# Kernel optimization log

Measured on AMD Instinct MI355X. Metric: run time of the kernel, lower is better.

Reference implementation:

```python
import jax, jax.numpy as jnp
import numpy as np

KB, KI = 6, 0   # kernel quantizer: quantized_bits(6, 0, alpha=1)
BB, BI = 6, 0   # bias quantizer:   quantized_bits(6, 0, alpha=1)
AB, AI = 6, 0   # activation:       quantized_relu(6, 0)


def _round_ste(p):
    # straight-through round (QKeras _round_through); tf.round and jnp.round
    # both round half-to-even
    return p + jax.lax.stop_gradient(jnp.round(p) - p)


def quantized_bits(x, bits, integer):
    # QKeras quantized_bits with keep_negative=1, symmetric=0, alpha=1
    m = float(2 ** (bits - 1))      # non-sign levels
    m_i = float(2 ** integer)
    p = x * (m / m_i)
    return (m_i / m) * jnp.clip(_round_ste(p), -m, m - 1.0)


def quantized_relu(x, bits, integer):
    # QKeras quantized_relu with negative_slope=0, use_sigmoid=0
    m = float(2 ** bits)
    m_i = float(2 ** integer)
    p = x * (m / m_i)
    return (m_i / m) * jnp.clip(_round_ste(p), 0.0, m - 1.0)


def setup_inputs() -> dict:
    key = jax.random.key(0)
    ks = jax.random.split(key, 9)
    dims = [128, 1024, 2048, 4096, 4096]
    inp = {"x": jax.random.normal(ks[0], (8192, dims[0]), dtype=jnp.float32)}
    for i in range(4):
        fan_in, fan_out = dims[i], dims[i + 1]
        scale = np.sqrt(2.0 / (fan_in + fan_out))  # glorot-ish scale
        inp[f"W{i}"] = jax.random.normal(ks[1 + 2 * i], (fan_in, fan_out), dtype=jnp.float32) * scale
        inp[f"b{i}"] = jax.random.normal(ks[2 + 2 * i], (fan_out,), dtype=jnp.float32) * 0.01
    return inp


def reference(x, W0, b0, W1, b1, W2, b2, W3, b3):
    Ws = [W0, W1, W2, W3]
    bs = [b0, b1, b2, b3]
    h = x
    for i in range(4):
        wq = quantized_bits(Ws[i], KB, KI)
        bq = quantized_bits(bs[i], BB, BI)
        h = jnp.dot(h, wq) + bq
        if i != 3:  # last layer has activation=None
            h = quantized_relu(h, AB, AI)
    return h
```

## Files before the change

### kernel.cpp

```cpp
#include <hip/hip_runtime.h>
#include <stdint.h>

typedef int v4i __attribute__((ext_vector_type(4)));

__device__ __forceinline__ float qlevel(float x) {
  float p = rintf(x * 32.0f);
  return fminf(fmaxf(p, -32.0f), 31.0f);
}

__device__ __forceinline__ int8_t qrelu_level(float p) {
  int q = (int)rintf(p);
  q = q < 0 ? 0 : (q > 63 ? 63 : q);
  return (int8_t)q;
}

__device__ __forceinline__ void async16(const void* g, void* l) {
  __builtin_amdgcn_global_load_lds(
      (const __attribute__((address_space(1))) void*)g,
      (__attribute__((address_space(3))) void*)l, 16, 0, 0);
}

__global__ __launch_bounds__(256) void quant_w0_k(const float* __restrict__ W,
                                                  int8_t* __restrict__ wq) {
  int i = blockIdx.x * 256 + threadIdx.x;
  float4 v = ((const float4*)W)[i];
  char4 c;
  c.x = (int8_t)(int)qlevel(v.x);
  c.y = (int8_t)(int)qlevel(v.y);
  c.z = (int8_t)(int)qlevel(v.z);
  c.w = (int8_t)(int)qlevel(v.w);
  ((char4*)wq)[i] = c;
}

__global__ __launch_bounds__(256) void quantT_k(const float* __restrict__ W,
                                                int8_t* __restrict__ wt,
                                                int K, int N) {
  const int t = threadIdx.x;
  const int l = t & 63;
  const int kc = t >> 6;
  const int k0 = blockIdx.y * 64 + kc * 16;
  const int n = blockIdx.x * 64 + l;
  union { int8_t b[16]; int4 v; } u;
#pragma unroll
  for (int j = 0; j < 16; ++j)
    u.b[j] = (int8_t)(int)qlevel(W[(size_t)(k0 + j) * N + n]);
  *(int4*)&wt[(size_t)n * K + k0] = u.v;
}

__global__ __launch_bounds__(256) void quant_bias_k(
    const float* __restrict__ b0, const float* __restrict__ b1,
    const float* __restrict__ b2, const float* __restrict__ b3,
    float* __restrict__ o0, float* __restrict__ o1,
    float* __restrict__ o2, float* __restrict__ o3) {
  int i = blockIdx.x * 256 + threadIdx.x;
  if (i < 1024) o0[i] = qlevel(b0[i]);
  if (i < 2048) o1[i] = qlevel(b1[i]);
  o2[i] = qlevel(b2[i]);
  o3[i] = qlevel(b3[i]);
}

__global__ __launch_bounds__(256) void layer0_k(const float* __restrict__ x,
                                                const int8_t* __restrict__ w0q,
                                                const float* __restrict__ bint,
                                                int8_t* __restrict__ a1) {
  const int K = 128, N = 1024;
  __shared__ float xs[64][132];
  __shared__ int8_t wsm[128][64];
  const int tid = threadIdx.x;
  const int m0 = blockIdx.y * 64;
  const int n0 = blockIdx.x * 64;
#pragma unroll
  for (int i = 0; i < 8; ++i) {
    int idx = tid + 256 * i;
    int row = idx >> 5, c4 = idx & 31;
    float4 v = *(const float4*)(x + (size_t)(m0 + row) * K + c4 * 4);
    *(float4*)&xs[row][c4 * 4] = v;
  }
#pragma unroll
  for (int i = 0; i < 8; ++i) {
    int idx = tid + 256 * i;
    int k = idx >> 4, c4 = idx & 15;
    *(int*)&wsm[k][c4 * 4] = *(const int*)(w0q + (size_t)k * N + n0 + c4 * 4);
  }
  __syncthreads();
  const int ty = tid >> 4, tx = tid & 15;
  float acc[4][4] = {};
  for (int k4 = 0; k4 < K; k4 += 4) {
    float xr[4][4];
#pragma unroll
    for (int i = 0; i < 4; ++i) {
      float4 v = *(const float4*)&xs[ty * 4 + i][k4];
      xr[i][0] = v.x; xr[i][1] = v.y; xr[i][2] = v.z; xr[i][3] = v.w;
    }
#pragma unroll
    for (int kk = 0; kk < 4; ++kk) {
      char4 cv = *(const char4*)&wsm[k4 + kk][tx * 4];
      float w0 = (float)cv.x, w1 = (float)cv.y, w2 = (float)cv.z, w3 = (float)cv.w;
#pragma unroll
      for (int i = 0; i < 4; ++i) {
        acc[i][0] = fmaf(xr[i][kk], w0, acc[i][0]);
        acc[i][1] = fmaf(xr[i][kk], w1, acc[i][1]);
        acc[i][2] = fmaf(xr[i][kk], w2, acc[i][2]);
        acc[i][3] = fmaf(xr[i][kk], w3, acc[i][3]);
      }
    }
  }
  const int n = n0 + tx * 4;
  float b0v = 2.0f * bint[n + 0], b1v = 2.0f * bint[n + 1];
  float b2v = 2.0f * bint[n + 2], b3v = 2.0f * bint[n + 3];
#pragma unroll
  for (int i = 0; i < 4; ++i) {
    int m = m0 + ty * 4 + i;
    char4 o;
    o.x = qrelu_level(2.0f * acc[i][0] + b0v);
    o.y = qrelu_level(2.0f * acc[i][1] + b1v);
    o.z = qrelu_level(2.0f * acc[i][2] + b2v);
    o.w = qrelu_level(2.0f * acc[i][3] + b3v);
    *(char4*)&a1[(size_t)m * 1024 + n] = o;
  }
}

template <bool FINAL>
__global__ __launch_bounds__(512) void gemm_i8(const int8_t* __restrict__ A,
                                               const int8_t* __restrict__ BT,
                                               const float* __restrict__ bint,
                                               void* __restrict__ outp,
                                               int M, int N, int K) {
  __shared__ __align__(16) int8_t ldsA[3][256 * 64];
  __shared__ __align__(16) int8_t ldsB[3][256 * 64];
  const int tid = threadIdx.x;
  const int wid = tid >> 6;
  const int lane = tid & 63;
  const int wm = wid >> 2, wn = wid & 3;
  const int quad = lane >> 4, r = lane & 15;
  const int m0 = blockIdx.y * 256, n0 = blockIdx.x * 256;

  const int8_t* Ab = A + (size_t)m0 * K;
  const int8_t* Bb = BT + (size_t)n0 * K;

  const int srow = tid >> 2;
  const int sp = tid & 3;
  const int skc = (sp - (srow >> 1)) & 3;
  const int8_t* gA0 = Ab + (size_t)srow * K + skc * 16;
  const int8_t* gA1 = Ab + (size_t)(srow + 128) * K + skc * 16;
  const int8_t* gB0 = Bb + (size_t)srow * K + skc * 16;
  const int8_t* gB1 = Bb + (size_t)(srow + 128) * K + skc * 16;
  const int ldsOff0 = (wid * 64) * 16;
  const int ldsOff1 = (512 + wid * 64) * 16;

  const int pfrag = (quad + (r >> 1)) & 3;

  v4i acc[8][4] = {};

#define STAGE_A(buf, kt)                              \
  do {                                                \
    async16(gA0 + (kt) * 64, &ldsA[buf][ldsOff0]);    \
    async16(gA1 + (kt) * 64, &ldsA[buf][ldsOff1]);    \
  } while (0)
#define STAGE_B(buf, kt)                              \
  do {                                                \
    async16(gB0 + (kt) * 64, &ldsB[buf][ldsOff0]);    \
    async16(gB1 + (kt) * 64, &ldsB[buf][ldsOff1]);    \
  } while (0)

#define ITER(p, q, kt, doStage, vmN)                                          \
  do {                                                                        \
    v4i bf[4], af[4];                                                         \
    const int8_t* La_ = &ldsA[p][0];                                          \
    const int8_t* Lb_ = &ldsB[p][0];                                          \
    _Pragma("unroll")                                                         \
    for (int nt = 0; nt < 4; ++nt)                                            \
      bf[nt] = *(const v4i*)&Lb_[(wn * 64 + nt * 16 + r) * 64 + pfrag * 16];  \
    _Pragma("unroll")                                                         \
    for (int mt = 0; mt < 4; ++mt)                                            \
      af[mt] = *(const v4i*)&La_[(wm * 128 + mt * 16 + r) * 64 + pfrag * 16]; \
    if (doStage) STAGE_A(q, kt);                                              \
    __builtin_amdgcn_s_barrier();                                             \
    asm volatile("s_waitcnt lgkmcnt(0)" ::: "memory");                        \
    __builtin_amdgcn_sched_barrier(0);                                        \
    __builtin_amdgcn_s_setprio(1);                                            \
    _Pragma("unroll")                                                         \
    for (int mt = 0; mt < 4; ++mt)                                            \
      _Pragma("unroll")                                                       \
      for (int nt = 0; nt < 4; ++nt)                                          \
        acc[mt][nt] = __builtin_amdgcn_mfma_i32_16x16x64_i8(                  \
            af[mt], bf[nt], acc[mt][nt], 0, 0, 0);                            \
    __builtin_amdgcn_s_setprio(0);                                            \
    __builtin_amdgcn_s_barrier();                                             \
    _Pragma("unroll")                                                         \
    for (int mt = 0; mt < 4; ++mt)                                            \
      af[mt] = *(const v4i*)&La_[(wm * 128 + 64 + mt * 16 + r) * 64 +         \
                                 pfrag * 16];                                 \
    if (doStage) STAGE_B(q, kt);                                              \
    if (vmN == 4) asm volatile("s_waitcnt vmcnt(4)" ::: "memory");            \
    if (vmN == 0) asm volatile("s_waitcnt vmcnt(0)" ::: "memory");            \
    __builtin_amdgcn_s_barrier();                                             \
    asm volatile("s_waitcnt lgkmcnt(0)" ::: "memory");                        \
    __builtin_amdgcn_sched_barrier(0);                                        \
    __builtin_amdgcn_s_setprio(1);                                            \
    _Pragma("unroll")                                                         \
    for (int mt = 0; mt < 4; ++mt)                                            \
      _Pragma("unroll")                                                       \
      for (int nt = 0; nt < 4; ++nt)                                          \
        acc[4 + mt][nt] = __builtin_amdgcn_mfma_i32_16x16x64_i8(              \
            af[mt], bf[nt], acc[4 + mt][nt], 0, 0, 0);                        \
    __builtin_amdgcn_s_setprio(0);                                            \
    __builtin_amdgcn_s_barrier();                                             \
  } while (0)

  const int NT = K >> 6;

  STAGE_A(0, 0); STAGE_B(0, 0);
  STAGE_A(1, 1); STAGE_B(1, 1);
  asm volatile("s_waitcnt vmcnt(4)" ::: "memory");
  __builtin_amdgcn_s_barrier();

  for (int t = 0; t < NT - 2; ++t) {
    ITER(t % 3, (t + 2) % 3, t + 2, true, 4);
  }
  ITER((NT - 2) % 3, 0, 0, false, 0);
  ITER((NT - 1) % 3, 0, 0, false, -1);

#undef ITER
#undef STAGE_A
#undef STAGE_B

  const int mbase = m0 + wm * 128;
  const int nbase = n0 + wn * 64;
  if (FINAL) {
    float* out = (float*)outp;
#pragma unroll
    for (int nt = 0; nt < 4; ++nt) {
      int n = nbase + nt * 16 + r;
      float bq = bint[n] * 0.03125f;
#pragma unroll
      for (int mt = 0; mt < 8; ++mt)
#pragma unroll
        for (int g = 0; g < 4; ++g) {
          int m = mbase + mt * 16 + quad * 4 + g;
          out[(size_t)m * N + n] = (float)acc[mt][nt][g] * (1.0f / 2048.0f) + bq;
        }
    }
  } else {
    int8_t* out = (int8_t*)outp;
#pragma unroll
    for (int nt = 0; nt < 4; ++nt) {
      int n = nbase + nt * 16 + r;
      float b2 = 2.0f * bint[n];
#pragma unroll
      for (int mt = 0; mt < 8; ++mt)
#pragma unroll
        for (int g = 0; g < 4; ++g) {
          int m = mbase + mt * 16 + quad * 4 + g;
          out[(size_t)m * N + n] =
              qrelu_level((float)acc[mt][nt][g] * 0.03125f + b2);
        }
    }
  }
}

extern "C" void kernel_launch(void* const* d_in, const int* in_sizes, int n_in,
                              void* d_out, int out_size, void* d_ws, size_t ws_size,
                              hipStream_t stream) {
  const float* x  = (const float*)d_in[0];
  const float* W0 = (const float*)d_in[1];
  const float* b0 = (const float*)d_in[2];
  const float* W1 = (const float*)d_in[3];
  const float* b1 = (const float*)d_in[4];
  const float* W2 = (const float*)d_in[5];
  const float* b2 = (const float*)d_in[6];
  const float* W3 = (const float*)d_in[7];
  const float* b3 = (const float*)d_in[8];

  uint8_t* ws = (uint8_t*)d_ws;
  int8_t* wq0 = (int8_t*)(ws + 0);
  int8_t* wt1 = (int8_t*)(ws + 131072);
  int8_t* wt2 = (int8_t*)(ws + 2228224);
  int8_t* wt3 = (int8_t*)(ws + 10616832);
  float*  bq0 = (float*)(ws + 27394048);
  float*  bq1 = (float*)(ws + 27398144);
  float*  bq2 = (float*)(ws + 27406336);
  float*  bq3 = (float*)(ws + 27422720);
  int8_t* a1  = (int8_t*)(ws + 27439104);
  int8_t* a2  = (int8_t*)(ws + 35827712);
  int8_t* a3  = (int8_t*)(ws + 52604928);

  quant_w0_k<<<128, 256, 0, stream>>>(W0, wq0);
  quantT_k<<<dim3(2048 / 64, 1024 / 64), 256, 0, stream>>>(W1, wt1, 1024, 2048);
  quantT_k<<<dim3(4096 / 64, 2048 / 64), 256, 0, stream>>>(W2, wt2, 2048, 4096);
  quantT_k<<<dim3(4096 / 64, 4096 / 64), 256, 0, stream>>>(W3, wt3, 4096, 4096);
  quant_bias_k<<<16, 256, 0, stream>>>(b0, b1, b2, b3, bq0, bq1, bq2, bq3);
  layer0_k<<<dim3(16, 128), 256, 0, stream>>>(x, wq0, bq0, a1);
  gemm_i8<false><<<dim3(2048 / 256, 8192 / 256), 512, 0, stream>>>(
      a1, wt1, bq1, a2, 8192, 2048, 1024);
  gemm_i8<false><<<dim3(4096 / 256, 8192 / 256), 512, 0, stream>>>(
      a2, wt2, bq2, a3, 8192, 4096, 2048);
  gemm_i8<true><<<dim3(4096 / 256, 8192 / 256), 512, 0, stream>>>(
      a3, wt3, bq3, d_out, 8192, 4096, 4096);
}
```

Before: 492.6 us.

## Collapse per-iteration barriers into one barrier and load all A fragments upfront

Each k-step of the int8 MFMA GEMM main loop now runs behind a single barrier instead of four. All eight A fragments and the four B fragments are read from LDS before any MFMA, and the A and B async global-to-LDS copies for the next stage are issued together. The explicit lgkmcnt waits and sched_barriers go away, so the compiler places the LDS waits and can overlap the LDS reads with the MFMAs. The goal is to cut barrier stalls and wave synchronisation per k-step. The cost is extra registers for the second A fragment set and less explicit control over where instructions are scheduled.

```diff
diff --git a/kernel.cpp b/kernel.cpp
--- a/kernel.cpp
+++ b/kernel.cpp
@@ -152,20 +152,18 @@
 
   v4i acc[8][4] = {};
 
-#define STAGE_A(buf, kt)                              \
+#define STAGE(buf, kt)                                \
   do {                                                \
     async16(gA0 + (kt) * 64, &ldsA[buf][ldsOff0]);    \
     async16(gA1 + (kt) * 64, &ldsA[buf][ldsOff1]);    \
-  } while (0)
-#define STAGE_B(buf, kt)                              \
-  do {                                                \
     async16(gB0 + (kt) * 64, &ldsB[buf][ldsOff0]);    \
     async16(gB1 + (kt) * 64, &ldsB[buf][ldsOff1]);    \
   } while (0)
 
 #define ITER(p, q, kt, doStage, vmN)                                          \
   do {                                                                        \
-    v4i bf[4], af[4];                                                         \
+    __builtin_amdgcn_s_barrier();                                             \
+    v4i bf[4], af0[4], af1[4];                                                \
     const int8_t* La_ = &ldsA[p][0];                                          \
     const int8_t* Lb_ = &ldsB[p][0];                                          \
     _Pragma("unroll")                                                         \
@@ -173,47 +171,35 @@
       bf[nt] = *(const v4i*)&Lb_[(wn * 64 + nt * 16 + r) * 64 + pfrag * 16];  \
     _Pragma("unroll")                                                         \
     for (int mt = 0; mt < 4; ++mt)                                            \
-      af[mt] = *(const v4i*)&La_[(wm * 128 + mt * 16 + r) * 64 + pfrag * 16]; \
-    if (doStage) STAGE_A(q, kt);                                              \
-    __builtin_amdgcn_s_barrier();                                             \
-    asm volatile("s_waitcnt lgkmcnt(0)" ::: "memory");                        \
-    __builtin_amdgcn_sched_barrier(0);                                        \
+      af0[mt] = *(const v4i*)&La_[(wm * 128 + mt * 16 + r) * 64 + pfrag * 16];\
+    _Pragma("unroll")                                                         \
+    for (int mt = 0; mt < 4; ++mt)                                            \
+      af1[mt] = *(const v4i*)&La_[(wm * 128 + 64 + mt * 16 + r) * 64 +        \
+                                  pfrag * 16];                                \
+    if (doStage) STAGE(q, kt);                                                \
     __builtin_amdgcn_s_setprio(1);                                            \
     _Pragma("unroll")                                                         \
     for (int mt = 0; mt < 4; ++mt)                                            \
       _Pragma("unroll")                                                       \
       for (int nt = 0; nt < 4; ++nt)                                          \
         acc[mt][nt] = __builtin_amdgcn_mfma_i32_16x16x64_i8(                  \
-            af[mt], bf[nt], acc[mt][nt], 0, 0, 0);                            \
-    __builtin_amdgcn_s_setprio(0);                                            \
-    __builtin_amdgcn_s_barrier();                                             \
-    _Pragma("unroll")                                                         \
-    for (int mt = 0; mt < 4; ++mt)                                            \
-      af[mt] = *(const v4i*)&La_[(wm * 128 + 64 + mt * 16 + r) * 64 +         \
-                                 pfrag * 16];                                 \
-    if (doStage) STAGE_B(q, kt);                                              \
-    if (vmN == 4) asm volatile("s_waitcnt vmcnt(4)" ::: "memory");            \
-    if (vmN == 0) asm volatile("s_waitcnt vmcnt(0)" ::: "memory");            \
-    __builtin_amdgcn_s_barrier();                                             \
-    asm volatile("s_waitcnt lgkmcnt(0)" ::: "memory");                        \
-    __builtin_amdgcn_sched_barrier(0);                                        \
-    __builtin_amdgcn_s_setprio(1);                                            \
+            af0[mt], bf[nt], acc[mt][nt], 0, 0, 0);                           \
     _Pragma("unroll")                                                         \
     for (int mt = 0; mt < 4; ++mt)                                            \
       _Pragma("unroll")                                                       \
       for (int nt = 0; nt < 4; ++nt)                                          \
         acc[4 + mt][nt] = __builtin_amdgcn_mfma_i32_16x16x64_i8(              \
-            af[mt], bf[nt], acc[4 + mt][nt], 0, 0, 0);                        \
+            af1[mt], bf[nt], acc[4 + mt][nt], 0, 0, 0);                       \
     __builtin_amdgcn_s_setprio(0);                                            \
-    __builtin_amdgcn_s_barrier();                                             \
+    if (vmN == 4) asm volatile("s_waitcnt vmcnt(4)" ::: "memory");            \
+    if (vmN == 0) asm volatile("s_waitcnt vmcnt(0)" ::: "memory");            \
   } while (0)
 
   const int NT = K >> 6;
 
-  STAGE_A(0, 0); STAGE_B(0, 0);
-  STAGE_A(1, 1); STAGE_B(1, 1);
+  STAGE(0, 0);
+  STAGE(1, 1);
   asm volatile("s_waitcnt vmcnt(4)" ::: "memory");
-  __builtin_amdgcn_s_barrier();
 
   for (int t = 0; t < NT - 2; ++t) {
     ITER(t % 3, (t + 2) % 3, t + 2, true, 4);
@@ -222,8 +208,7 @@
   ITER((NT - 1) % 3, 0, 0, false, -1);
 
 #undef ITER
-#undef STAGE_A
-#undef STAGE_B
+#undef STAGE
 
   const int mbase = m0 + wm * 128;
   const int nbase = n0 + wn * 64;
```

Result: faster. 459.8 us (-6.7%).
